# Optimization experiments

Hardware: AMD Instinct MI355X
Metric: run time of the kernel (lower is better)

The kernel has to match this reference:

```python
import jax, jax.numpy as jnp
import numpy as np
import math

IN_DIM = 3
N_LEVELS = 16
F = 2
LOG2_T = 19
T = 2 ** LOG2_T
BASE_RES = 16
FINEST_RES = 512
N_POINTS = 1048576

# Per-level resolutions (static, matches torch buffer construction)
_b = math.exp((math.log(FINEST_RES) - math.log(BASE_RES)) / max(N_LEVELS - 1, 1))
RES = np.array([int(BASE_RES * _b ** i) for i in range(N_LEVELS)], dtype=np.int32)  # [L]
# XOR spatial-hash primes (dim 0 uses prime 1)
PRIMES = np.array([1, 2654435761, 805459861, 3674653429], dtype=np.uint32)


def _hash(coords_u32):
    """coords_u32: (..., IN_DIM) uint32 -> int32 hash in [0, T).
    uint32 wraparound arithmetic gives the same low-19 bits as torch's int64
    math, since T divides 2**32 and XOR/product low bits are self-contained."""
    h = coords_u32[..., 0]
    for d in range(1, IN_DIM):
        h = h ^ (coords_u32[..., d] * PRIMES[d % len(PRIMES)])
    return (h & jnp.uint32(T - 1)).astype(jnp.int32)


def setup_inputs() -> dict:
    key = jax.random.key(0)
    k1, k2 = jax.random.split(key)
    x = jax.random.uniform(k1, (N_POINTS, IN_DIM), dtype=jnp.float32)  # coords in [0,1]
    embeddings = jax.random.uniform(
        k2, (N_LEVELS, T, F), minval=-1e-4, maxval=1e-4, dtype=jnp.float32
    )
    return {"x": x, "embeddings": embeddings}


def reference(x, embeddings):
    N = x.shape[0]
    res_f = jnp.asarray(RES, dtype=x.dtype)            # [L]
    res_i = jnp.asarray(RES, dtype=jnp.int32)          # [L]

    # Scale all levels at once: [L, N, D]
    x_scaled = x[None, :, :] * (res_f[:, None, None] - 1.0)
    x_floor = jnp.clip(x_scaled.astype(jnp.int32), 0, res_i[:, None, None] - 2)
    x_frac = x_scaled - x_floor.astype(x.dtype)        # [L, N, D]

    feat = jnp.zeros((N_LEVELS, N, F), dtype=x.dtype)
    for corner in range(2 ** IN_DIM):                  # fixed 8 corners
        off = np.array([(corner >> d) & 1 for d in range(IN_DIM)], dtype=np.int32)
        corner_coords = jnp.clip(x_floor + off, 0, res_i[:, None, None] - 1)
        h = _hash(corner_coords.astype(jnp.uint32))    # [L, N]
        # gather per-level features: embeddings[l, h[l, n]] -> [L, N, F]
        corner_feat = jnp.take_along_axis(embeddings, h[:, :, None], axis=1)
        # N-linear weight: prod over dims of frac or (1-frac)
        w = jnp.prod(
            jnp.where(off.astype(bool), x_frac, 1.0 - x_frac),
            axis=-1, keepdims=True,
        )                                              # [L, N, 1]
        feat = feat + w * corner_feat

    # concat levels along feature dim: [N, L*F]
    return jnp.moveaxis(feat, 0, 1).reshape(N, N_LEVELS * F)
```

## Files before the change

### kernel.cpp

```cpp
#include <hip/hip_runtime.h>
#include <math.h>
#include <stdint.h>

#define LOG2_T 19
#define T_SIZE (1u << LOG2_T)
#define T_MASK (T_SIZE - 1u)
#define N_LEVELS 16
#define N_DENSE 8
#define PRIME1 2654435761u
#define PRIME2 805459861u

typedef unsigned long long u64;
typedef float f4v __attribute__((ext_vector_type(4)));

struct Params {
    int res[N_LEVELS];
    int brick[N_DENSE];
    int off[N_DENSE];
    int dense_total;
};

__device__ __forceinline__ float bf_lo(uint32_t v) { return __uint_as_float(v << 16); }
__device__ __forceinline__ float bf_hi(uint32_t v) { return __uint_as_float(v & 0xFFFF0000u); }

__device__ __forceinline__ uint32_t f32_to_bf16_rne(float f) {
    uint32_t u = __float_as_uint(f);
    u += 0x7FFFu + ((u >> 16) & 1u);
    return u >> 16;
}
__device__ __forceinline__ uint32_t pack2(float2 e) {
    return f32_to_bf16_rne(e.x) | (f32_to_bf16_rne(e.y) << 16);
}

__device__ __forceinline__ void nt_store_f2(float2 v, float2* p) {
    union { float2 f; u64 u; } cv; cv.f = v;
    __builtin_nontemporal_store(cv.u, (u64*)p);
}
__device__ __forceinline__ float2 nt_load_f2(const float2* p) {
    union { float2 f; u64 u; } cv;
    cv.u = __builtin_nontemporal_load((const u64*)p);
    return cv.f;
}

__device__ __forceinline__ void pair_load(const uint32_t* __restrict__ t,
                                          uint32_t h0, uint32_t& e0, uint32_t& e1) {
    const uint2 q = *(const uint2*)(t + (h0 & ~1u));
    const bool hi = (h0 & 1u);
    e0 = hi ? q.y : q.x;
    e1 = hi ? q.x : q.y;
}

__global__ __launch_bounds__(256) void hg_build_fine(
    const float2* __restrict__ emb, uint32_t* __restrict__ tabF)
{
    const int i = blockIdx.x * 256 + threadIdx.x;
    tabF[i] = pack2(emb[(size_t)N_DENSE * T_SIZE + i]);
}

__global__ __launch_bounds__(256) void hg_build_dense(
    const float2* __restrict__ emb, uint32_t* __restrict__ tabD, Params P)
{
    const int i = blockIdx.x * 256 + threadIdx.x;
    if (i >= P.dense_total) return;
    int l = 0;
    while (l < N_DENSE - 1 && i >= P.off[l + 1]) ++l;
    const int e = i - P.off[l];
    const int B = P.brick[l], R = P.res[l];
    const int sub = e & 7, br = e >> 3;
    int bx = br % B; int t2 = br / B; int by = t2 % B; int bz = t2 / B;
    int x = bx * 2 + (sub & 1);        if (x > R - 1) x = R - 1;
    int y = by * 2 + ((sub >> 1) & 1); if (y > R - 1) y = R - 1;
    int z = bz * 2 + (sub >> 2);       if (z > R - 1) z = R - 1;
    const uint32_t h = ((uint32_t)x ^ ((uint32_t)y * PRIME1) ^ ((uint32_t)z * PRIME2)) & T_MASK;
    tabD[i] = pack2(emb[(size_t)l * T_SIZE + h]);
}

struct Pt { int ix, iy, iz; float fx, fy, fz; };

__device__ __forceinline__ Pt mk_pt(float x0, float x1, float x2,
                                    int rl, float rf) {
    Pt p;
    const float sx = x0 * rf, sy = x1 * rf, sz = x2 * rf;
    int ix = (int)sx; ix = ix < 0 ? 0 : (ix > rl - 2 ? rl - 2 : ix);
    int iy = (int)sy; iy = iy < 0 ? 0 : (iy > rl - 2 ? rl - 2 : iy);
    int iz = (int)sz; iz = iz < 0 ? 0 : (iz > rl - 2 ? rl - 2 : iz);
    p.ix = ix; p.iy = iy; p.iz = iz;
    p.fx = sx - (float)ix; p.fy = sy - (float)iy; p.fz = sz - (float)iz;
    return p;
}

__device__ __forceinline__ void gather_fine(const uint32_t* __restrict__ t,
                                            const Pt& p, uint32_t c[8]) {
    const uint32_t hx0 = (uint32_t)p.ix;
    const uint32_t hy0 = (uint32_t)p.iy * PRIME1, hy1 = hy0 + PRIME1;
    const uint32_t hz0 = (uint32_t)p.iz * PRIME2, hz1 = hz0 + PRIME2;
    const uint32_t n00 = hy0 ^ hz0, n10 = hy1 ^ hz0, n01 = hy0 ^ hz1, n11 = hy1 ^ hz1;
    if ((p.ix & 1) == 0) {
        pair_load(t, (hx0 ^ n00) & T_MASK, c[0], c[1]);
        pair_load(t, (hx0 ^ n10) & T_MASK, c[2], c[3]);
        pair_load(t, (hx0 ^ n01) & T_MASK, c[4], c[5]);
        pair_load(t, (hx0 ^ n11) & T_MASK, c[6], c[7]);
    } else {
        const uint32_t hx1 = hx0 + 1u;
        c[0] = t[(hx0 ^ n00) & T_MASK]; c[1] = t[(hx1 ^ n00) & T_MASK];
        c[2] = t[(hx0 ^ n10) & T_MASK]; c[3] = t[(hx1 ^ n10) & T_MASK];
        c[4] = t[(hx0 ^ n01) & T_MASK]; c[5] = t[(hx1 ^ n01) & T_MASK];
        c[6] = t[(hx0 ^ n11) & T_MASK]; c[7] = t[(hx1 ^ n11) & T_MASK];
    }
}

__device__ __forceinline__ void gather_dense(const uint32_t* __restrict__ t,
                                             int B, const Pt& p, uint32_t c[8]) {
    const int ix = p.ix, iy = p.iy, iz = p.iz;
    const int bx0 = ix >> 1, sx0 = ix & 1;
    const int by0 = iy >> 1, sy0 = iy & 1, by1 = (iy + 1) >> 1, sy1 = (iy + 1) & 1;
    const int bz0 = iz >> 1, sz0 = iz & 1, bz1 = (iz + 1) >> 1, sz1 = (iz + 1) & 1;
    const int zy00 = (((bz0 * B + by0) * B) << 3) | (sy0 << 1) | (sz0 << 2);
    const int zy10 = (((bz0 * B + by1) * B) << 3) | (sy1 << 1) | (sz0 << 2);
    const int zy01 = (((bz1 * B + by0) * B) << 3) | (sy0 << 1) | (sz1 << 2);
    const int zy11 = (((bz1 * B + by1) * B) << 3) | (sy1 << 1) | (sz1 << 2);
    if (sx0 == 0) {
        if (sy0 == 0) {
            const uint4 q0 = *(const uint4*)(t + zy00 + (bx0 << 3));
            const uint4 q1 = *(const uint4*)(t + zy01 + (bx0 << 3));
            c[0] = q0.x; c[1] = q0.y; c[2] = q0.z; c[3] = q0.w;
            c[4] = q1.x; c[5] = q1.y; c[6] = q1.z; c[7] = q1.w;
        } else {
            const uint2 q0 = *(const uint2*)(t + zy00 + (bx0 << 3));
            const uint2 q1 = *(const uint2*)(t + zy10 + (bx0 << 3));
            const uint2 q2 = *(const uint2*)(t + zy01 + (bx0 << 3));
            const uint2 q3 = *(const uint2*)(t + zy11 + (bx0 << 3));
            c[0] = q0.x; c[1] = q0.y; c[2] = q1.x; c[3] = q1.y;
            c[4] = q2.x; c[5] = q2.y; c[6] = q3.x; c[7] = q3.y;
        }
    } else {
        const int bx1 = bx0 + 1;
        c[0] = t[zy00 + (bx0 << 3) + 1]; c[1] = t[zy00 + (bx1 << 3)];
        c[2] = t[zy10 + (bx0 << 3) + 1]; c[3] = t[zy10 + (bx1 << 3)];
        c[4] = t[zy01 + (bx0 << 3) + 1]; c[5] = t[zy01 + (bx1 << 3)];
        c[6] = t[zy11 + (bx0 << 3) + 1]; c[7] = t[zy11 + (bx1 << 3)];
    }
}

__device__ __forceinline__ float2 blend8(const uint32_t c[8], const Pt& p) {
    const float wx0 = 1.0f - p.fx, wx1 = p.fx;
    const float wy0 = 1.0f - p.fy, wy1 = p.fy;
    const float wz0 = 1.0f - p.fz, wz1 = p.fz;
    float w, f0 = 0.0f, f1 = 0.0f;
    w = wx0 * wy0 * wz0; f0 = fmaf(w, bf_lo(c[0]), f0); f1 = fmaf(w, bf_hi(c[0]), f1);
    w = wx1 * wy0 * wz0; f0 = fmaf(w, bf_lo(c[1]), f0); f1 = fmaf(w, bf_hi(c[1]), f1);
    w = wx0 * wy1 * wz0; f0 = fmaf(w, bf_lo(c[2]), f0); f1 = fmaf(w, bf_hi(c[2]), f1);
    w = wx1 * wy1 * wz0; f0 = fmaf(w, bf_lo(c[3]), f0); f1 = fmaf(w, bf_hi(c[3]), f1);
    w = wx0 * wy0 * wz1; f0 = fmaf(w, bf_lo(c[4]), f0); f1 = fmaf(w, bf_hi(c[4]), f1);
    w = wx1 * wy0 * wz1; f0 = fmaf(w, bf_lo(c[5]), f0); f1 = fmaf(w, bf_hi(c[5]), f1);
    w = wx0 * wy1 * wz1; f0 = fmaf(w, bf_lo(c[6]), f0); f1 = fmaf(w, bf_hi(c[6]), f1);
    w = wx1 * wy1 * wz1; f0 = fmaf(w, bf_lo(c[7]), f0); f1 = fmaf(w, bf_hi(c[7]), f1);
    float2 o; o.x = f0; o.y = f1;
    return o;
}

__global__ __launch_bounds__(256, 4) void hg_levels(
    const float* __restrict__ x,
    const uint32_t* __restrict__ tabF,
    const uint32_t* __restrict__ tabD,
    float2* __restrict__ feat,
    int N, Params P)
{
    const int l  = blockIdx.x & 7;
    const int lf = l + 8;
    const int n0 = (blockIdx.x >> 3) * 512 + threadIdx.x;
    if (n0 >= N) return;
    const int n1 = n0 + 256;
    const bool hasB = (n1 < N);
    const int nB = hasB ? n1 : n0;

    const float xa0 = x[n0 * 3 + 0], xa1 = x[n0 * 3 + 1], xa2 = x[n0 * 3 + 2];
    const float xb0 = x[nB * 3 + 0], xb1 = x[nB * 3 + 1], xb2 = x[nB * 3 + 2];

    const int   rd  = P.res[l];  const float rdf = (float)(rd - 1);
    const int   rfi = P.res[lf]; const float rff = (float)(rfi - 1);

    const Pt fA = mk_pt(xa0, xa1, xa2, rfi, rff);
    const Pt fB = mk_pt(xb0, xb1, xb2, rfi, rff);
    const Pt dA = mk_pt(xa0, xa1, xa2, rd, rdf);
    const Pt dB = mk_pt(xb0, xb1, xb2, rd, rdf);

    uint32_t cfA[8], cfB[8], cdA[8], cdB[8];
    const uint32_t* __restrict__ tf = tabF + (size_t)l * T_SIZE;
    gather_fine(tf, fA, cfA);
    gather_fine(tf, fB, cfB);
    const uint32_t* __restrict__ td = tabD + P.off[l];
    const int B = P.brick[l];
    gather_dense(td, B, dA, cdA);
    gather_dense(td, B, dB, cdB);

    __builtin_amdgcn_sched_barrier(0);

    const float2 oFA = blend8(cfA, fA);
    const float2 oFB = blend8(cfB, fB);
    const float2 oDA = blend8(cdA, dA);
    const float2 oDB = blend8(cdB, dB);

    nt_store_f2(oDA, &feat[(size_t)l  * N + n0]);
    nt_store_f2(oFA, &feat[(size_t)lf * N + n0]);
    if (hasB) {
        nt_store_f2(oDB, &feat[(size_t)l  * N + n1]);
        nt_store_f2(oFB, &feat[(size_t)lf * N + n1]);
    }
}

__global__ __launch_bounds__(256) void hg_transpose(
    const float2* __restrict__ feat, f4v* __restrict__ out, int N)
{
    __shared__ float2 st[N_LEVELS][33];
    const int base = blockIdx.x * 32;
    const int t = threadIdx.x;
#pragma unroll
    for (int i = 0; i < 2; ++i) {
        const int idx = i * 256 + t;
        const int l = idx >> 5, p = idx & 31;
        const int n = base + p;
        st[l][p] = (n < N) ? nt_load_f2(&feat[(size_t)l * N + n]) : make_float2(0.f, 0.f);
    }
    __syncthreads();
    const int p = t >> 3, k = t & 7;
    const int n = base + p;
    if (n < N) {
        const float2 a = st[2 * k][p], b = st[2 * k + 1][p];
        f4v o; o.x = a.x; o.y = a.y; o.z = b.x; o.w = b.y;
        __builtin_nontemporal_store(o, &out[(size_t)n * 8 + k]);
    }
}

__global__ __launch_bounds__(256) void hg_fallback(
    const float* __restrict__ x, const float* __restrict__ emb,
    float* __restrict__ out, int N, Params P)
{
    const int gid = blockIdx.x * 256 + threadIdx.x;
    const int n = gid >> 4, l = gid & 15;
    if (n >= N) return;
    const int rl = P.res[l];
    const float rf = (float)(rl - 1);
    float sx = x[n * 3 + 0] * rf, sy = x[n * 3 + 1] * rf, sz = x[n * 3 + 2] * rf;
    int ix = (int)sx; ix = ix < 0 ? 0 : (ix > rl - 2 ? rl - 2 : ix);
    int iy = (int)sy; iy = iy < 0 ? 0 : (iy > rl - 2 ? rl - 2 : iy);
    int iz = (int)sz; iz = iz < 0 ? 0 : (iz > rl - 2 ? rl - 2 : iz);
    const float fx = sx - ix, fy = sy - iy, fz = sz - iz;
    const uint32_t hx0 = (uint32_t)ix, hx1 = hx0 + 1u;
    const uint32_t hy0 = (uint32_t)iy * PRIME1, hy1 = hy0 + PRIME1;
    const uint32_t hz0 = (uint32_t)iz * PRIME2, hz1 = hz0 + PRIME2;
    const float2* tab = (const float2*)emb + (size_t)l * T_SIZE;
    float2 e0 = tab[(hx0 ^ hy0 ^ hz0) & T_MASK], e1 = tab[(hx1 ^ hy0 ^ hz0) & T_MASK];
    float2 e2 = tab[(hx0 ^ hy1 ^ hz0) & T_MASK], e3 = tab[(hx1 ^ hy1 ^ hz0) & T_MASK];
    float2 e4 = tab[(hx0 ^ hy0 ^ hz1) & T_MASK], e5 = tab[(hx1 ^ hy0 ^ hz1) & T_MASK];
    float2 e6 = tab[(hx0 ^ hy1 ^ hz1) & T_MASK], e7 = tab[(hx1 ^ hy1 ^ hz1) & T_MASK];
    const float wx0 = 1.0f - fx, wx1 = fx, wy0 = 1.0f - fy, wy1 = fy, wz0 = 1.0f - fz, wz1 = fz;
    float w, f0 = 0.0f, f1 = 0.0f;
    w = wx0 * wy0 * wz0; f0 = fmaf(w, e0.x, f0); f1 = fmaf(w, e0.y, f1);
    w = wx1 * wy0 * wz0; f0 = fmaf(w, e1.x, f0); f1 = fmaf(w, e1.y, f1);
    w = wx0 * wy1 * wz0; f0 = fmaf(w, e2.x, f0); f1 = fmaf(w, e2.y, f1);
    w = wx1 * wy1 * wz0; f0 = fmaf(w, e3.x, f0); f1 = fmaf(w, e3.y, f1);
    w = wx0 * wy0 * wz1; f0 = fmaf(w, e4.x, f0); f1 = fmaf(w, e4.y, f1);
    w = wx1 * wy0 * wz1; f0 = fmaf(w, e5.x, f0); f1 = fmaf(w, e5.y, f1);
    w = wx0 * wy1 * wz1; f0 = fmaf(w, e6.x, f0); f1 = fmaf(w, e6.y, f1);
    w = wx1 * wy1 * wz1; f0 = fmaf(w, e7.x, f0); f1 = fmaf(w, e7.y, f1);
    float2 o; o.x = f0; o.y = f1;
    ((float2*)out)[(size_t)n * N_LEVELS + l] = o;
}

extern "C" void kernel_launch(void* const* d_in, const int* in_sizes, int n_in,
                              void* d_out, int out_size, void* d_ws, size_t ws_size,
                              hipStream_t stream) {
    const float* x   = (const float*)d_in[0];
    const float* emb = (const float*)d_in[1];
    const int N = in_sizes[0] / 3;

    Params P;
    const double b = exp((log(512.0) - log(16.0)) / 15.0);
    for (int i = 0; i < N_LEVELS; ++i)
        P.res[i] = (int)(16.0 * pow(b, (double)i));
    int acc = 0;
    for (int i = 0; i < N_DENSE; ++i) {
        P.brick[i] = (P.res[i] + 1) >> 1;
        P.off[i] = acc;
        acc += P.brick[i] * P.brick[i] * P.brick[i] * 8;
    }
    P.dense_total = acc;

    const size_t fine_bytes  = (size_t)N_DENSE * T_SIZE * sizeof(uint32_t);
    const size_t dense_bytes = ((size_t)acc * sizeof(uint32_t) + 255) & ~255ull;
    const size_t feat_bytes  = (size_t)N_LEVELS * N * sizeof(float2);

    if (ws_size >= fine_bytes + dense_bytes + feat_bytes) {
        uint32_t* tabF = (uint32_t*)d_ws;
        uint32_t* tabD = (uint32_t*)((char*)d_ws + fine_bytes);
        float2*   feat = (float2*)((char*)d_ws + fine_bytes + dense_bytes);

        hipLaunchKernelGGL(hg_build_fine, dim3(N_DENSE * T_SIZE / 256), dim3(256), 0, stream,
                           (const float2*)emb, tabF);
        hipLaunchKernelGGL(hg_build_dense, dim3((P.dense_total + 255) / 256), dim3(256), 0, stream,
                           (const float2*)emb, tabD, P);

        const int chunks = (N + 511) / 512;
        hipLaunchKernelGGL(hg_levels, dim3(chunks * 8), dim3(256), 0, stream,
                           x, tabF, tabD, feat, N, P);

        hipLaunchKernelGGL(hg_transpose, dim3((N + 31) / 32), dim3(256), 0, stream,
                           feat, (f4v*)d_out, N);
    } else {
        hipLaunchKernelGGL(hg_fallback, dim3((N * 16 + 255) / 256), dim3(256), 0, stream,
                           x, emb, (float*)d_out, N, P);
    }
}
```

Measured before the change: 519.0 us.

## Use per-cell and x-pair dense tables, quad-aligned hashed loads, vectorized I/O

Replaces the 2x2x2 brick dense layout with two schemes. The five coarsest levels store all 8 corners per cell contiguously, so each point needs two 16-byte loads. The next three levels store x-adjacent pairs per row, so each point needs four 8-byte loads. Fine hashed levels now load an aligned uint4 around each hash and pull the x+1 neighbour from it when the XOR delta stays inside the quad, with separate scalar loads otherwise. Each thread now handles two adjacent points, so x loads and feature stores become vectorized. The cost is larger precomputed tables (about 8x duplication for coarse levels) and an extra build kernel.

```diff
diff --git a/kernel.cpp b/kernel.cpp
--- a/kernel.cpp
+++ b/kernel.cpp
@@ -7,6 +7,7 @@
 #define T_MASK (T_SIZE - 1u)
 #define N_LEVELS 16
 #define N_DENSE 8
+#define N_CELL 5
 #define PRIME1 2654435761u
 #define PRIME2 805459861u
 
@@ -15,9 +16,11 @@
 
 struct Params {
     int res[N_LEVELS];
-    int brick[N_DENSE];
-    int off[N_DENSE];
-    int dense_total;
+    int dOff[N_DENSE];
+    int cellOffC[N_CELL + 1];
+    int pairOffE[4];
+    int cellTot;
+    int pairTot;
 };
 
 __device__ __forceinline__ float bf_lo(uint32_t v) { return __uint_as_float(v << 16); }
@@ -42,12 +45,10 @@
     return cv.f;
 }
 
-__device__ __forceinline__ void pair_load(const uint32_t* __restrict__ t,
-                                          uint32_t h0, uint32_t& e0, uint32_t& e1) {
-    const uint2 q = *(const uint2*)(t + (h0 & ~1u));
-    const bool hi = (h0 & 1u);
-    e0 = hi ? q.y : q.x;
-    e1 = hi ? q.x : q.y;
+__device__ __forceinline__ uint32_t sel4(uint4 q, uint32_t s) {
+    const uint32_t a = (s & 1u) ? q.y : q.x;
+    const uint32_t b = (s & 1u) ? q.w : q.z;
+    return (s & 2u) ? b : a;
 }
 
 __global__ __launch_bounds__(256) void hg_build_fine(
@@ -57,22 +58,42 @@
     tabF[i] = pack2(emb[(size_t)N_DENSE * T_SIZE + i]);
 }
 
-__global__ __launch_bounds__(256) void hg_build_dense(
+__global__ __launch_bounds__(256) void hg_build_cell(
     const float2* __restrict__ emb, uint32_t* __restrict__ tabD, Params P)
 {
     const int i = blockIdx.x * 256 + threadIdx.x;
-    if (i >= P.dense_total) return;
+    if (i >= P.cellTot * 8) return;
+    const int cg = i >> 3, k = i & 7;
     int l = 0;
-    while (l < N_DENSE - 1 && i >= P.off[l + 1]) ++l;
-    const int e = i - P.off[l];
-    const int B = P.brick[l], R = P.res[l];
-    const int sub = e & 7, br = e >> 3;
-    int bx = br % B; int t2 = br / B; int by = t2 % B; int bz = t2 / B;
-    int x = bx * 2 + (sub & 1);        if (x > R - 1) x = R - 1;
-    int y = by * 2 + ((sub >> 1) & 1); if (y > R - 1) y = R - 1;
-    int z = bz * 2 + (sub >> 2);       if (z > R - 1) z = R - 1;
-    const uint32_t h = ((uint32_t)x ^ ((uint32_t)y * PRIME1) ^ ((uint32_t)z * PRIME2)) & T_MASK;
-    tabD[i] = pack2(emb[(size_t)l * T_SIZE + h]);
+    while (l < N_CELL - 1 && cg >= P.cellOffC[l + 1]) ++l;
+    const int e = cg - P.cellOffC[l];
+    const int C = P.res[l] - 1;
+    const int ix = e % C; const int r = e / C; const int iy = r % C; const int iz = r / C;
+    const uint32_t xx = (uint32_t)(ix + (k & 1));
+    const uint32_t yy = (uint32_t)(iy + ((k >> 1) & 1));
+    const uint32_t zz = (uint32_t)(iz + (k >> 2));
+    const uint32_t h = (xx ^ (yy * PRIME1) ^ (zz * PRIME2)) & T_MASK;
+    tabD[P.dOff[l] + e * 8 + k] = pack2(emb[(size_t)l * T_SIZE + h]);
+}
+
+__global__ __launch_bounds__(256) void hg_build_pair(
+    const float2* __restrict__ emb, uint32_t* __restrict__ tabD, Params P)
+{
+    const int j = blockIdx.x * 256 + threadIdx.x;
+    if (j >= P.pairTot) return;
+    int lp = 0;
+    while (lp < 2 && j >= P.pairOffE[lp + 1]) ++lp;
+    const int e = j - P.pairOffE[lp];
+    const int l = lp + N_CELL;
+    const int R = P.res[l], C = R - 1;
+    const int ix = e % C; const int r = e / C; const int yc = r % R; const int zc = r / R;
+    const uint32_t m = (((uint32_t)yc) * PRIME1) ^ (((uint32_t)zc) * PRIME2);
+    const uint32_t h0 = (((uint32_t)ix)      ^ m) & T_MASK;
+    const uint32_t h1 = (((uint32_t)ix + 1u) ^ m) & T_MASK;
+    uint2 v;
+    v.x = pack2(emb[(size_t)l * T_SIZE + h0]);
+    v.y = pack2(emb[(size_t)l * T_SIZE + h1]);
+    *(uint2*)(tabD + P.dOff[l] + (size_t)e * 2) = v;
 }
 
 struct Pt { int ix, iy, iz; float fx, fy, fz; };
@@ -89,72 +110,23 @@
     return p;
 }
 
-__device__ __forceinline__ void gather_fine(const uint32_t* __restrict__ t,
-                                            const Pt& p, uint32_t c[8]) {
-    const uint32_t hx0 = (uint32_t)p.ix;
-    const uint32_t hy0 = (uint32_t)p.iy * PRIME1, hy1 = hy0 + PRIME1;
-    const uint32_t hz0 = (uint32_t)p.iz * PRIME2, hz1 = hz0 + PRIME2;
-    const uint32_t n00 = hy0 ^ hz0, n10 = hy1 ^ hz0, n01 = hy0 ^ hz1, n11 = hy1 ^ hz1;
-    if ((p.ix & 1) == 0) {
-        pair_load(t, (hx0 ^ n00) & T_MASK, c[0], c[1]);
-        pair_load(t, (hx0 ^ n10) & T_MASK, c[2], c[3]);
-        pair_load(t, (hx0 ^ n01) & T_MASK, c[4], c[5]);
-        pair_load(t, (hx0 ^ n11) & T_MASK, c[6], c[7]);
-    } else {
-        const uint32_t hx1 = hx0 + 1u;
-        c[0] = t[(hx0 ^ n00) & T_MASK]; c[1] = t[(hx1 ^ n00) & T_MASK];
-        c[2] = t[(hx0 ^ n10) & T_MASK]; c[3] = t[(hx1 ^ n10) & T_MASK];
-        c[4] = t[(hx0 ^ n01) & T_MASK]; c[5] = t[(hx1 ^ n01) & T_MASK];
-        c[6] = t[(hx0 ^ n11) & T_MASK]; c[7] = t[(hx1 ^ n11) & T_MASK];
-    }
-}
-
-__device__ __forceinline__ void gather_dense(const uint32_t* __restrict__ t,
-                                             int B, const Pt& p, uint32_t c[8]) {
-    const int ix = p.ix, iy = p.iy, iz = p.iz;
-    const int bx0 = ix >> 1, sx0 = ix & 1;
-    const int by0 = iy >> 1, sy0 = iy & 1, by1 = (iy + 1) >> 1, sy1 = (iy + 1) & 1;
-    const int bz0 = iz >> 1, sz0 = iz & 1, bz1 = (iz + 1) >> 1, sz1 = (iz + 1) & 1;
-    const int zy00 = (((bz0 * B + by0) * B) << 3) | (sy0 << 1) | (sz0 << 2);
-    const int zy10 = (((bz0 * B + by1) * B) << 3) | (sy1 << 1) | (sz0 << 2);
-    const int zy01 = (((bz1 * B + by0) * B) << 3) | (sy0 << 1) | (sz1 << 2);
-    const int zy11 = (((bz1 * B + by1) * B) << 3) | (sy1 << 1) | (sz1 << 2);
-    if (sx0 == 0) {
-        if (sy0 == 0) {
-            const uint4 q0 = *(const uint4*)(t + zy00 + (bx0 << 3));
-            const uint4 q1 = *(const uint4*)(t + zy01 + (bx0 << 3));
-            c[0] = q0.x; c[1] = q0.y; c[2] = q0.z; c[3] = q0.w;
-            c[4] = q1.x; c[5] = q1.y; c[6] = q1.z; c[7] = q1.w;
-        } else {
-            const uint2 q0 = *(const uint2*)(t + zy00 + (bx0 << 3));
-            const uint2 q1 = *(const uint2*)(t + zy10 + (bx0 << 3));
-            const uint2 q2 = *(const uint2*)(t + zy01 + (bx0 << 3));
-            const uint2 q3 = *(const uint2*)(t + zy11 + (bx0 << 3));
-            c[0] = q0.x; c[1] = q0.y; c[2] = q1.x; c[3] = q1.y;
-            c[4] = q2.x; c[5] = q2.y; c[6] = q3.x; c[7] = q3.y;
-        }
-    } else {
-        const int bx1 = bx0 + 1;
-        c[0] = t[zy00 + (bx0 << 3) + 1]; c[1] = t[zy00 + (bx1 << 3)];
-        c[2] = t[zy10 + (bx0 << 3) + 1]; c[3] = t[zy10 + (bx1 << 3)];
-        c[4] = t[zy01 + (bx0 << 3) + 1]; c[5] = t[zy01 + (bx1 << 3)];
-        c[6] = t[zy11 + (bx0 << 3) + 1]; c[7] = t[zy11 + (bx1 << 3)];
-    }
-}
-
-__device__ __forceinline__ float2 blend8(const uint32_t c[8], const Pt& p) {
-    const float wx0 = 1.0f - p.fx, wx1 = p.fx;
-    const float wy0 = 1.0f - p.fy, wy1 = p.fy;
-    const float wz0 = 1.0f - p.fz, wz1 = p.fz;
+__device__ __forceinline__ float2 blend8s(
+    uint32_t c0, uint32_t c1, uint32_t c2, uint32_t c3,
+    uint32_t c4, uint32_t c5, uint32_t c6, uint32_t c7,
+    float fx, float fy, float fz)
+{
+    const float wx0 = 1.0f - fx, wx1 = fx;
+    const float wy0 = 1.0f - fy, wy1 = fy;
+    const float wz0 = 1.0f - fz, wz1 = fz;
     float w, f0 = 0.0f, f1 = 0.0f;
-    w = wx0 * wy0 * wz0; f0 = fmaf(w, bf_lo(c[0]), f0); f1 = fmaf(w, bf_hi(c[0]), f1);
-    w = wx1 * wy0 * wz0; f0 = fmaf(w, bf_lo(c[1]), f0); f1 = fmaf(w, bf_hi(c[1]), f1);
-    w = wx0 * wy1 * wz0; f0 = fmaf(w, bf_lo(c[2]), f0); f1 = fmaf(w, bf_hi(c[2]), f1);
-    w = wx1 * wy1 * wz0; f0 = fmaf(w, bf_lo(c[3]), f0); f1 = fmaf(w, bf_hi(c[3]), f1);
-    w = wx0 * wy0 * wz1; f0 = fmaf(w, bf_lo(c[4]), f0); f1 = fmaf(w, bf_hi(c[4]), f1);
-    w = wx1 * wy0 * wz1; f0 = fmaf(w, bf_lo(c[5]), f0); f1 = fmaf(w, bf_hi(c[5]), f1);
-    w = wx0 * wy1 * wz1; f0 = fmaf(w, bf_lo(c[6]), f0); f1 = fmaf(w, bf_hi(c[6]), f1);
-    w = wx1 * wy1 * wz1; f0 = fmaf(w, bf_lo(c[7]), f0); f1 = fmaf(w, bf_hi(c[7]), f1);
+    w = wx0 * wy0 * wz0; f0 = fmaf(w, bf_lo(c0), f0); f1 = fmaf(w, bf_hi(c0), f1);
+    w = wx1 * wy0 * wz0; f0 = fmaf(w, bf_lo(c1), f0); f1 = fmaf(w, bf_hi(c1), f1);
+    w = wx0 * wy1 * wz0; f0 = fmaf(w, bf_lo(c2), f0); f1 = fmaf(w, bf_hi(c2), f1);
+    w = wx1 * wy1 * wz0; f0 = fmaf(w, bf_lo(c3), f0); f1 = fmaf(w, bf_hi(c3), f1);
+    w = wx0 * wy0 * wz1; f0 = fmaf(w, bf_lo(c4), f0); f1 = fmaf(w, bf_hi(c4), f1);
+    w = wx1 * wy0 * wz1; f0 = fmaf(w, bf_lo(c5), f0); f1 = fmaf(w, bf_hi(c5), f1);
+    w = wx0 * wy1 * wz1; f0 = fmaf(w, bf_lo(c6), f0); f1 = fmaf(w, bf_hi(c6), f1);
+    w = wx1 * wy1 * wz1; f0 = fmaf(w, bf_lo(c7), f0); f1 = fmaf(w, bf_hi(c7), f1);
     float2 o; o.x = f0; o.y = f1;
     return o;
 }
@@ -168,44 +140,148 @@
 {
     const int l  = blockIdx.x & 7;
     const int lf = l + 8;
-    const int n0 = (blockIdx.x >> 3) * 512 + threadIdx.x;
+    const int tt = (blockIdx.x >> 3) * 256 + threadIdx.x;
+    const int n0 = tt * 2;
     if (n0 >= N) return;
-    const int n1 = n0 + 256;
+    const int n1 = n0 + 1;
     const bool hasB = (n1 < N);
-    const int nB = hasB ? n1 : n0;
-
-    const float xa0 = x[n0 * 3 + 0], xa1 = x[n0 * 3 + 1], xa2 = x[n0 * 3 + 2];
-    const float xb0 = x[nB * 3 + 0], xb1 = x[nB * 3 + 1], xb2 = x[nB * 3 + 2];
-
-    const int   rd  = P.res[l];  const float rdf = (float)(rd - 1);
-    const int   rfi = P.res[lf]; const float rff = (float)(rfi - 1);
-
-    const Pt fA = mk_pt(xa0, xa1, xa2, rfi, rff);
-    const Pt fB = mk_pt(xb0, xb1, xb2, rfi, rff);
-    const Pt dA = mk_pt(xa0, xa1, xa2, rd, rdf);
-    const Pt dB = mk_pt(xb0, xb1, xb2, rd, rdf);
-
-    uint32_t cfA[8], cfB[8], cdA[8], cdB[8];
+
+    float ax, ay, az, bx, by, bz;
+    const float* xb = x + (size_t)n0 * 3;
+    if (hasB) {
+        const float2 u0 = *(const float2*)(xb);
+        const float2 u1 = *(const float2*)(xb + 2);
+        const float2 u2 = *(const float2*)(xb + 4);
+        ax = u0.x; ay = u0.y; az = u1.x; bx = u1.y; by = u2.x; bz = u2.y;
+    } else {
+        ax = xb[0]; ay = xb[1]; az = xb[2]; bx = ax; by = ay; bz = az;
+    }
+
+    const int rd = P.res[l];  const float rdf = (float)(rd - 1);
+    const int rf = P.res[lf]; const float rff = (float)(rf - 1);
+
+    const Pt fA = mk_pt(ax, ay, az, rf, rff);
+    const Pt fB = mk_pt(bx, by, bz, rf, rff);
+    const Pt dA = mk_pt(ax, ay, az, rd, rdf);
+    const Pt dB = mk_pt(bx, by, bz, rd, rdf);
+
     const uint32_t* __restrict__ tf = tabF + (size_t)l * T_SIZE;
-    gather_fine(tf, fA, cfA);
-    gather_fine(tf, fB, cfB);
-    const uint32_t* __restrict__ td = tabD + P.off[l];
-    const int B = P.brick[l];
-    gather_dense(td, B, dA, cdA);
-    gather_dense(td, B, dB, cdB);
+
+    const uint32_t hxA = (uint32_t)fA.ix;
+    const uint32_t dxA = hxA ^ (hxA + 1u);
+    const uint32_t yA0 = (uint32_t)fA.iy * PRIME1, yA1 = yA0 + PRIME1;
+    const uint32_t zA0 = (uint32_t)fA.iz * PRIME2, zA1 = zA0 + PRIME2;
+    const uint32_t iA00 = (hxA ^ yA0 ^ zA0) & T_MASK;
+    const uint32_t iA10 = (hxA ^ yA1 ^ zA0) & T_MASK;
+    const uint32_t iA01 = (hxA ^ yA0 ^ zA1) & T_MASK;
+    const uint32_t iA11 = (hxA ^ yA1 ^ zA1) & T_MASK;
+    const uint4 qA00 = *(const uint4*)(tf + (iA00 & ~3u));
+    const uint4 qA10 = *(const uint4*)(tf + (iA10 & ~3u));
+    const uint4 qA01 = *(const uint4*)(tf + (iA01 & ~3u));
+    const uint4 qA11 = *(const uint4*)(tf + (iA11 & ~3u));
+
+    const uint32_t hxB = (uint32_t)fB.ix;
+    const uint32_t dxB = hxB ^ (hxB + 1u);
+    const uint32_t yB0 = (uint32_t)fB.iy * PRIME1, yB1 = yB0 + PRIME1;
+    const uint32_t zB0 = (uint32_t)fB.iz * PRIME2, zB1 = zB0 + PRIME2;
+    const uint32_t iB00 = (hxB ^ yB0 ^ zB0) & T_MASK;
+    const uint32_t iB10 = (hxB ^ yB1 ^ zB0) & T_MASK;
+    const uint32_t iB01 = (hxB ^ yB0 ^ zB1) & T_MASK;
+    const uint32_t iB11 = (hxB ^ yB1 ^ zB1) & T_MASK;
+    const uint4 qB00 = *(const uint4*)(tf + (iB00 & ~3u));
+    const uint4 qB10 = *(const uint4*)(tf + (iB10 & ~3u));
+    const uint4 qB01 = *(const uint4*)(tf + (iB01 & ~3u));
+    const uint4 qB11 = *(const uint4*)(tf + (iB11 & ~3u));
+
+    uint32_t eA1 = 0, eA3 = 0, eA5 = 0, eA7 = 0;
+    const bool exA = dxA >= 4u;
+    if (exA) {
+        eA1 = tf[(iA00 ^ dxA) & T_MASK];
+        eA3 = tf[(iA10 ^ dxA) & T_MASK];
+        eA5 = tf[(iA01 ^ dxA) & T_MASK];
+        eA7 = tf[(iA11 ^ dxA) & T_MASK];
+    }
+    uint32_t eB1 = 0, eB3 = 0, eB5 = 0, eB7 = 0;
+    const bool exB = dxB >= 4u;
+    if (exB) {
+        eB1 = tf[(iB00 ^ dxB) & T_MASK];
+        eB3 = tf[(iB10 ^ dxB) & T_MASK];
+        eB5 = tf[(iB01 ^ dxB) & T_MASK];
+        eB7 = tf[(iB11 ^ dxB) & T_MASK];
+    }
+
+    uint32_t a0, a1, a2, a3, a4, a5, a6, a7;
+    uint32_t b0, b1, b2, b3, b4, b5, b6, b7;
+    if (l < N_CELL) {
+        const int C = rd - 1;
+        const uint32_t* cbA = tabD + P.dOff[l] + (size_t)((dA.iz * C + dA.iy) * C + dA.ix) * 8;
+        const uint4 qa0 = *(const uint4*)cbA;
+        const uint4 qa1 = *(const uint4*)(cbA + 4);
+        const uint32_t* cbB = tabD + P.dOff[l] + (size_t)((dB.iz * C + dB.iy) * C + dB.ix) * 8;
+        const uint4 qb0 = *(const uint4*)cbB;
+        const uint4 qb1 = *(const uint4*)(cbB + 4);
+        a0 = qa0.x; a1 = qa0.y; a2 = qa0.z; a3 = qa0.w;
+        a4 = qa1.x; a5 = qa1.y; a6 = qa1.z; a7 = qa1.w;
+        b0 = qb0.x; b1 = qb0.y; b2 = qb0.z; b3 = qb0.w;
+        b4 = qb1.x; b5 = qb1.y; b6 = qb1.z; b7 = qb1.w;
+    } else {
+        const int R = rd, C = rd - 1;
+        const uint32_t* pb = tabD + P.dOff[l];
+        const int rA0 = (dA.iz * R + dA.iy) * C + dA.ix;
+        const int rA1 = rA0 + C;
+        const int rA2 = rA0 + R * C;
+        const int rA3 = rA2 + C;
+        const uint2 pA0 = *(const uint2*)(pb + (size_t)rA0 * 2);
+        const uint2 pA1 = *(const uint2*)(pb + (size_t)rA1 * 2);
+        const uint2 pA2 = *(const uint2*)(pb + (size_t)rA2 * 2);
+        const uint2 pA3 = *(const uint2*)(pb + (size_t)rA3 * 2);
+        const int rB0 = (dB.iz * R + dB.iy) * C + dB.ix;
+        const int rB1 = rB0 + C;
+        const int rB2 = rB0 + R * C;
+        const int rB3 = rB2 + C;
+        const uint2 pB0 = *(const uint2*)(pb + (size_t)rB0 * 2);
+        const uint2 pB1 = *(const uint2*)(pb + (size_t)rB1 * 2);
+        const uint2 pB2 = *(const uint2*)(pb + (size_t)rB2 * 2);
+        const uint2 pB3 = *(const uint2*)(pb + (size_t)rB3 * 2);
+        a0 = pA0.x; a1 = pA0.y; a2 = pA1.x; a3 = pA1.y;
+        a4 = pA2.x; a5 = pA2.y; a6 = pA3.x; a7 = pA3.y;
+        b0 = pB0.x; b1 = pB0.y; b2 = pB1.x; b3 = pB1.y;
+        b4 = pB2.x; b5 = pB2.y; b6 = pB3.x; b7 = pB3.y;
+    }
 
     __builtin_amdgcn_sched_barrier(0);
 
-    const float2 oFA = blend8(cfA, fA);
-    const float2 oFB = blend8(cfB, fB);
-    const float2 oDA = blend8(cdA, dA);
-    const float2 oDB = blend8(cdB, dB);
-
-    nt_store_f2(oDA, &feat[(size_t)l  * N + n0]);
-    nt_store_f2(oFA, &feat[(size_t)lf * N + n0]);
+    const uint32_t fA0 = sel4(qA00, iA00 & 3u);
+    const uint32_t fA1 = exA ? eA1 : sel4(qA00, (iA00 ^ dxA) & 3u);
+    const uint32_t fA2 = sel4(qA10, iA10 & 3u);
+    const uint32_t fA3 = exA ? eA3 : sel4(qA10, (iA10 ^ dxA) & 3u);
+    const uint32_t fA4 = sel4(qA01, iA01 & 3u);
+    const uint32_t fA5 = exA ? eA5 : sel4(qA01, (iA01 ^ dxA) & 3u);
+    const uint32_t fA6 = sel4(qA11, iA11 & 3u);
+    const uint32_t fA7 = exA ? eA7 : sel4(qA11, (iA11 ^ dxA) & 3u);
+
+    const uint32_t fB0 = sel4(qB00, iB00 & 3u);
+    const uint32_t fB1 = exB ? eB1 : sel4(qB00, (iB00 ^ dxB) & 3u);
+    const uint32_t fB2 = sel4(qB10, iB10 & 3u);
+    const uint32_t fB3 = exB ? eB3 : sel4(qB10, (iB10 ^ dxB) & 3u);
+    const uint32_t fB4 = sel4(qB01, iB01 & 3u);
+    const uint32_t fB5 = exB ? eB5 : sel4(qB01, (iB01 ^ dxB) & 3u);
+    const uint32_t fB6 = sel4(qB11, iB11 & 3u);
+    const uint32_t fB7 = exB ? eB7 : sel4(qB11, (iB11 ^ dxB) & 3u);
+
+    const float2 oFA = blend8s(fA0, fA1, fA2, fA3, fA4, fA5, fA6, fA7, fA.fx, fA.fy, fA.fz);
+    const float2 oFB = blend8s(fB0, fB1, fB2, fB3, fB4, fB5, fB6, fB7, fB.fx, fB.fy, fB.fz);
+    const float2 oDA = blend8s(a0, a1, a2, a3, a4, a5, a6, a7, dA.fx, dA.fy, dA.fz);
+    const float2 oDB = blend8s(b0, b1, b2, b3, b4, b5, b6, b7, dB.fx, dB.fy, dB.fz);
+
     if (hasB) {
-        nt_store_f2(oDB, &feat[(size_t)l  * N + n1]);
-        nt_store_f2(oFB, &feat[(size_t)lf * N + n1]);
+        f4v oD; oD.x = oDA.x; oD.y = oDA.y; oD.z = oDB.x; oD.w = oDB.y;
+        __builtin_nontemporal_store(oD, (f4v*)&feat[(size_t)l * N + n0]);
+        f4v oF; oF.x = oFA.x; oF.y = oFA.y; oF.z = oFB.x; oF.w = oFB.y;
+        __builtin_nontemporal_store(oF, (f4v*)&feat[(size_t)lf * N + n0]);
+    } else {
+        nt_store_f2(oDA, &feat[(size_t)l  * N + n0]);
+        nt_store_f2(oFA, &feat[(size_t)lf * N + n0]);
     }
 }
 
@@ -279,16 +355,25 @@
     const double b = exp((log(512.0) - log(16.0)) / 15.0);
     for (int i = 0; i < N_LEVELS; ++i)
         P.res[i] = (int)(16.0 * pow(b, (double)i));
-    int acc = 0;
-    for (int i = 0; i < N_DENSE; ++i) {
-        P.brick[i] = (P.res[i] + 1) >> 1;
-        P.off[i] = acc;
-        acc += P.brick[i] * P.brick[i] * P.brick[i] * 8;
-    }
-    P.dense_total = acc;
+
+    P.cellOffC[0] = 0;
+    for (int l = 0; l < N_CELL; ++l) {
+        const int C = P.res[l] - 1;
+        P.cellOffC[l + 1] = P.cellOffC[l] + C * C * C;
+    }
+    P.cellTot = P.cellOffC[N_CELL];
+    P.pairOffE[0] = 0;
+    for (int lp = 0; lp < 3; ++lp) {
+        const int R = P.res[N_CELL + lp], C = R - 1;
+        P.pairOffE[lp + 1] = P.pairOffE[lp] + C * R * R;
+    }
+    P.pairTot = P.pairOffE[3];
+    for (int l = 0; l < N_CELL; ++l) P.dOff[l] = P.cellOffC[l] * 8;
+    for (int lp = 0; lp < 3; ++lp)  P.dOff[N_CELL + lp] = P.cellTot * 8 + P.pairOffE[lp] * 2;
+    const size_t dense_dwords = (size_t)P.cellTot * 8 + (size_t)P.pairTot * 2;
 
     const size_t fine_bytes  = (size_t)N_DENSE * T_SIZE * sizeof(uint32_t);
-    const size_t dense_bytes = ((size_t)acc * sizeof(uint32_t) + 255) & ~255ull;
+    const size_t dense_bytes = (dense_dwords * sizeof(uint32_t) + 255) & ~255ull;
     const size_t feat_bytes  = (size_t)N_LEVELS * N * sizeof(float2);
 
     if (ws_size >= fine_bytes + dense_bytes + feat_bytes) {
@@ -298,7 +383,9 @@
 
         hipLaunchKernelGGL(hg_build_fine, dim3(N_DENSE * T_SIZE / 256), dim3(256), 0, stream,
                            (const float2*)emb, tabF);
-        hipLaunchKernelGGL(hg_build_dense, dim3((P.dense_total + 255) / 256), dim3(256), 0, stream,
+        hipLaunchKernelGGL(hg_build_cell, dim3((P.cellTot * 8 + 255) / 256), dim3(256), 0, stream,
+                           (const float2*)emb, tabD, P);
+        hipLaunchKernelGGL(hg_build_pair, dim3((P.pairTot + 255) / 256), dim3(256), 0, stream,
                            (const float2*)emb, tabD, P);
 
         const int chunks = (N + 511) / 512;
```

After: 614.3 us. +18.4%, slower.

## Replace brick dense tables with per-cell corner tables and quad-aligned hash gathers

Applied to the files above, without the earlier changes.

Only the coarsest 5 levels now get a dense table, and it stores all 8 corners of each cell contiguously, so a cell lookup is two 16-byte loads. The remaining 11 levels use a bf16 hash table read with 16-byte aligned quad loads that often cover both x-neighbours. Each thread now handles two adjacent points, which allows vectorised loads of x and 16-byte stores of features. The transpose tile grows to 128 points per block. The per-cell table duplicates corners about 8x and makes the build kernel larger, while the hash levels trade more bytes per load for fewer loads.

```diff
diff --git a/kernel.cpp b/kernel.cpp
--- a/kernel.cpp
+++ b/kernel.cpp
@@ -6,7 +6,8 @@
 #define T_SIZE (1u << LOG2_T)
 #define T_MASK (T_SIZE - 1u)
 #define N_LEVELS 16
-#define N_DENSE 8
+#define N_CELL 5
+#define N_HASH 11
 #define PRIME1 2654435761u
 #define PRIME2 805459861u
 
@@ -15,9 +16,9 @@
 
 struct Params {
     int res[N_LEVELS];
-    int brick[N_DENSE];
-    int off[N_DENSE];
-    int dense_total;
+    int dOff[N_CELL];
+    int cellOffC[N_CELL + 1];
+    int cellTot;
 };
 
 __device__ __forceinline__ float bf_lo(uint32_t v) { return __uint_as_float(v << 16); }
@@ -32,47 +33,45 @@
     return f32_to_bf16_rne(e.x) | (f32_to_bf16_rne(e.y) << 16);
 }
 
-__device__ __forceinline__ void nt_store_f2(float2 v, float2* p) {
-    union { float2 f; u64 u; } cv; cv.f = v;
-    __builtin_nontemporal_store(cv.u, (u64*)p);
-}
 __device__ __forceinline__ float2 nt_load_f2(const float2* p) {
     union { float2 f; u64 u; } cv;
     cv.u = __builtin_nontemporal_load((const u64*)p);
     return cv.f;
 }
-
-__device__ __forceinline__ void pair_load(const uint32_t* __restrict__ t,
-                                          uint32_t h0, uint32_t& e0, uint32_t& e1) {
-    const uint2 q = *(const uint2*)(t + (h0 & ~1u));
-    const bool hi = (h0 & 1u);
-    e0 = hi ? q.y : q.x;
-    e1 = hi ? q.x : q.y;
+__device__ __forceinline__ void nt_store_f2(float2 v, float2* p) {
+    union { float2 f; u64 u; } cv; cv.f = v;
+    __builtin_nontemporal_store(cv.u, (u64*)p);
+}
+
+__device__ __forceinline__ uint32_t sel4(uint4 q, uint32_t s) {
+    const uint32_t a = (s & 1u) ? q.y : q.x;
+    const uint32_t b = (s & 1u) ? q.w : q.z;
+    return (s & 2u) ? b : a;
 }
 
 __global__ __launch_bounds__(256) void hg_build_fine(
     const float2* __restrict__ emb, uint32_t* __restrict__ tabF)
 {
     const int i = blockIdx.x * 256 + threadIdx.x;
-    tabF[i] = pack2(emb[(size_t)N_DENSE * T_SIZE + i]);
-}
-
-__global__ __launch_bounds__(256) void hg_build_dense(
+    tabF[i] = pack2(emb[(size_t)N_CELL * T_SIZE + i]);
+}
+
+__global__ __launch_bounds__(256) void hg_build_cell(
     const float2* __restrict__ emb, uint32_t* __restrict__ tabD, Params P)
 {
     const int i = blockIdx.x * 256 + threadIdx.x;
-    if (i >= P.dense_total) return;
+    if (i >= P.cellTot * 8) return;
+    const int cg = i >> 3, k = i & 7;
     int l = 0;
-    while (l < N_DENSE - 1 && i >= P.off[l + 1]) ++l;
-    const int e = i - P.off[l];
-    const int B = P.brick[l], R = P.res[l];
-    const int sub = e & 7, br = e >> 3;
-    int bx = br % B; int t2 = br / B; int by = t2 % B; int bz = t2 / B;
-    int x = bx * 2 + (sub & 1);        if (x > R - 1) x = R - 1;
-    int y = by * 2 + ((sub >> 1) & 1); if (y > R - 1) y = R - 1;
-    int z = bz * 2 + (sub >> 2);       if (z > R - 1) z = R - 1;
-    const uint32_t h = ((uint32_t)x ^ ((uint32_t)y * PRIME1) ^ ((uint32_t)z * PRIME2)) & T_MASK;
-    tabD[i] = pack2(emb[(size_t)l * T_SIZE + h]);
+    while (l < N_CELL - 1 && cg >= P.cellOffC[l + 1]) ++l;
+    const int e = cg - P.cellOffC[l];
+    const int C = P.res[l] - 1;
+    const int ix = e % C; const int r = e / C; const int iy = r % C; const int iz = r / C;
+    const uint32_t xx = (uint32_t)(ix + (k & 1));
+    const uint32_t yy = (uint32_t)(iy + ((k >> 1) & 1));
+    const uint32_t zz = (uint32_t)(iz + (k >> 2));
+    const uint32_t h = (xx ^ (yy * PRIME1) ^ (zz * PRIME2)) & T_MASK;
+    tabD[P.dOff[l] + e * 8 + k] = pack2(emb[(size_t)l * T_SIZE + h]);
 }
 
 struct Pt { int ix, iy, iz; float fx, fy, fz; };
@@ -89,72 +88,65 @@
     return p;
 }
 
-__device__ __forceinline__ void gather_fine(const uint32_t* __restrict__ t,
-                                            const Pt& p, uint32_t c[8]) {
-    const uint32_t hx0 = (uint32_t)p.ix;
-    const uint32_t hy0 = (uint32_t)p.iy * PRIME1, hy1 = hy0 + PRIME1;
-    const uint32_t hz0 = (uint32_t)p.iz * PRIME2, hz1 = hz0 + PRIME2;
-    const uint32_t n00 = hy0 ^ hz0, n10 = hy1 ^ hz0, n01 = hy0 ^ hz1, n11 = hy1 ^ hz1;
-    if ((p.ix & 1) == 0) {
-        pair_load(t, (hx0 ^ n00) & T_MASK, c[0], c[1]);
-        pair_load(t, (hx0 ^ n10) & T_MASK, c[2], c[3]);
-        pair_load(t, (hx0 ^ n01) & T_MASK, c[4], c[5]);
-        pair_load(t, (hx0 ^ n11) & T_MASK, c[6], c[7]);
-    } else {
-        const uint32_t hx1 = hx0 + 1u;
-        c[0] = t[(hx0 ^ n00) & T_MASK]; c[1] = t[(hx1 ^ n00) & T_MASK];
-        c[2] = t[(hx0 ^ n10) & T_MASK]; c[3] = t[(hx1 ^ n10) & T_MASK];
-        c[4] = t[(hx0 ^ n01) & T_MASK]; c[5] = t[(hx1 ^ n01) & T_MASK];
-        c[6] = t[(hx0 ^ n11) & T_MASK]; c[7] = t[(hx1 ^ n11) & T_MASK];
-    }
-}
-
-__device__ __forceinline__ void gather_dense(const uint32_t* __restrict__ t,
-                                             int B, const Pt& p, uint32_t c[8]) {
-    const int ix = p.ix, iy = p.iy, iz = p.iz;
-    const int bx0 = ix >> 1, sx0 = ix & 1;
-    const int by0 = iy >> 1, sy0 = iy & 1, by1 = (iy + 1) >> 1, sy1 = (iy + 1) & 1;
-    const int bz0 = iz >> 1, sz0 = iz & 1, bz1 = (iz + 1) >> 1, sz1 = (iz + 1) & 1;
-    const int zy00 = (((bz0 * B + by0) * B) << 3) | (sy0 << 1) | (sz0 << 2);
-    const int zy10 = (((bz0 * B + by1) * B) << 3) | (sy1 << 1) | (sz0 << 2);
-    const int zy01 = (((bz1 * B + by0) * B) << 3) | (sy0 << 1) | (sz1 << 2);
-    const int zy11 = (((bz1 * B + by1) * B) << 3) | (sy1 << 1) | (sz1 << 2);
-    if (sx0 == 0) {
-        if (sy0 == 0) {
-            const uint4 q0 = *(const uint4*)(t + zy00 + (bx0 << 3));
-            const uint4 q1 = *(const uint4*)(t + zy01 + (bx0 << 3));
-            c[0] = q0.x; c[1] = q0.y; c[2] = q0.z; c[3] = q0.w;
-            c[4] = q1.x; c[5] = q1.y; c[6] = q1.z; c[7] = q1.w;
-        } else {
-            const uint2 q0 = *(const uint2*)(t + zy00 + (bx0 << 3));
-            const uint2 q1 = *(const uint2*)(t + zy10 + (bx0 << 3));
-            const uint2 q2 = *(const uint2*)(t + zy01 + (bx0 << 3));
-            const uint2 q3 = *(const uint2*)(t + zy11 + (bx0 << 3));
-            c[0] = q0.x; c[1] = q0.y; c[2] = q1.x; c[3] = q1.y;
-            c[4] = q2.x; c[5] = q2.y; c[6] = q3.x; c[7] = q3.y;
-        }
-    } else {
-        const int bx1 = bx0 + 1;
-        c[0] = t[zy00 + (bx0 << 3) + 1]; c[1] = t[zy00 + (bx1 << 3)];
-        c[2] = t[zy10 + (bx0 << 3) + 1]; c[3] = t[zy10 + (bx1 << 3)];
-        c[4] = t[zy01 + (bx0 << 3) + 1]; c[5] = t[zy01 + (bx1 << 3)];
-        c[6] = t[zy11 + (bx0 << 3) + 1]; c[7] = t[zy11 + (bx1 << 3)];
-    }
-}
-
-__device__ __forceinline__ float2 blend8(const uint32_t c[8], const Pt& p) {
+struct C8 { uint32_t c0, c1, c2, c3, c4, c5, c6, c7; };
+
+__device__ __forceinline__ C8 gather_hash(const uint32_t* __restrict__ t,
+                                          const Pt& p) {
+    const uint32_t hx = (uint32_t)p.ix;
+    const uint32_t dx = hx ^ (hx + 1u);
+    const uint32_t y0 = (uint32_t)p.iy * PRIME1, y1 = y0 + PRIME1;
+    const uint32_t z0 = (uint32_t)p.iz * PRIME2, z1 = z0 + PRIME2;
+    const uint32_t i00 = (hx ^ y0 ^ z0) & T_MASK;
+    const uint32_t i10 = (hx ^ y1 ^ z0) & T_MASK;
+    const uint32_t i01 = (hx ^ y0 ^ z1) & T_MASK;
+    const uint32_t i11 = (hx ^ y1 ^ z1) & T_MASK;
+    const uint4 q00 = *(const uint4*)(t + (i00 & ~3u));
+    const uint4 q10 = *(const uint4*)(t + (i10 & ~3u));
+    const uint4 q01 = *(const uint4*)(t + (i01 & ~3u));
+    const uint4 q11 = *(const uint4*)(t + (i11 & ~3u));
+    C8 r;
+    if (dx < 4u) {
+        r.c1 = sel4(q00, (i00 ^ dx) & 3u);
+        r.c3 = sel4(q10, (i10 ^ dx) & 3u);
+        r.c5 = sel4(q01, (i01 ^ dx) & 3u);
+        r.c7 = sel4(q11, (i11 ^ dx) & 3u);
+    } else {
+        r.c1 = t[(i00 ^ dx) & T_MASK];
+        r.c3 = t[(i10 ^ dx) & T_MASK];
+        r.c5 = t[(i01 ^ dx) & T_MASK];
+        r.c7 = t[(i11 ^ dx) & T_MASK];
+    }
+    r.c0 = sel4(q00, i00 & 3u);
+    r.c2 = sel4(q10, i10 & 3u);
+    r.c4 = sel4(q01, i01 & 3u);
+    r.c6 = sel4(q11, i11 & 3u);
+    return r;
+}
+
+__device__ __forceinline__ C8 gather_cell(const uint32_t* __restrict__ t,
+                                          int C, const Pt& p) {
+    const uint32_t* cb = t + (size_t)((p.iz * C + p.iy) * C + p.ix) * 8;
+    const uint4 q0 = *(const uint4*)cb;
+    const uint4 q1 = *(const uint4*)(cb + 4);
+    C8 r;
+    r.c0 = q0.x; r.c1 = q0.y; r.c2 = q0.z; r.c3 = q0.w;
+    r.c4 = q1.x; r.c5 = q1.y; r.c6 = q1.z; r.c7 = q1.w;
+    return r;
+}
+
+__device__ __forceinline__ float2 blend8(const C8& c, const Pt& p) {
     const float wx0 = 1.0f - p.fx, wx1 = p.fx;
     const float wy0 = 1.0f - p.fy, wy1 = p.fy;
     const float wz0 = 1.0f - p.fz, wz1 = p.fz;
     float w, f0 = 0.0f, f1 = 0.0f;
-    w = wx0 * wy0 * wz0; f0 = fmaf(w, bf_lo(c[0]), f0); f1 = fmaf(w, bf_hi(c[0]), f1);
-    w = wx1 * wy0 * wz0; f0 = fmaf(w, bf_lo(c[1]), f0); f1 = fmaf(w, bf_hi(c[1]), f1);
-    w = wx0 * wy1 * wz0; f0 = fmaf(w, bf_lo(c[2]), f0); f1 = fmaf(w, bf_hi(c[2]), f1);
-    w = wx1 * wy1 * wz0; f0 = fmaf(w, bf_lo(c[3]), f0); f1 = fmaf(w, bf_hi(c[3]), f1);
-    w = wx0 * wy0 * wz1; f0 = fmaf(w, bf_lo(c[4]), f0); f1 = fmaf(w, bf_hi(c[4]), f1);
-    w = wx1 * wy0 * wz1; f0 = fmaf(w, bf_lo(c[5]), f0); f1 = fmaf(w, bf_hi(c[5]), f1);
-    w = wx0 * wy1 * wz1; f0 = fmaf(w, bf_lo(c[6]), f0); f1 = fmaf(w, bf_hi(c[6]), f1);
-    w = wx1 * wy1 * wz1; f0 = fmaf(w, bf_lo(c[7]), f0); f1 = fmaf(w, bf_hi(c[7]), f1);
+    w = wx0 * wy0 * wz0; f0 = fmaf(w, bf_lo(c.c0), f0); f1 = fmaf(w, bf_hi(c.c0), f1);
+    w = wx1 * wy0 * wz0; f0 = fmaf(w, bf_lo(c.c1), f0); f1 = fmaf(w, bf_hi(c.c1), f1);
+    w = wx0 * wy1 * wz0; f0 = fmaf(w, bf_lo(c.c2), f0); f1 = fmaf(w, bf_hi(c.c2), f1);
+    w = wx1 * wy1 * wz0; f0 = fmaf(w, bf_lo(c.c3), f0); f1 = fmaf(w, bf_hi(c.c3), f1);
+    w = wx0 * wy0 * wz1; f0 = fmaf(w, bf_lo(c.c4), f0); f1 = fmaf(w, bf_hi(c.c4), f1);
+    w = wx1 * wy0 * wz1; f0 = fmaf(w, bf_lo(c.c5), f0); f1 = fmaf(w, bf_hi(c.c5), f1);
+    w = wx0 * wy1 * wz1; f0 = fmaf(w, bf_lo(c.c6), f0); f1 = fmaf(w, bf_hi(c.c6), f1);
+    w = wx1 * wy1 * wz1; f0 = fmaf(w, bf_lo(c.c7), f0); f1 = fmaf(w, bf_hi(c.c7), f1);
     float2 o; o.x = f0; o.y = f1;
     return o;
 }
@@ -168,67 +160,94 @@
 {
     const int l  = blockIdx.x & 7;
     const int lf = l + 8;
-    const int n0 = (blockIdx.x >> 3) * 512 + threadIdx.x;
+    const int tt = (blockIdx.x >> 3) * 256 + threadIdx.x;
+    const int n0 = tt * 2;
     if (n0 >= N) return;
-    const int n1 = n0 + 256;
+    const int n1 = n0 + 1;
     const bool hasB = (n1 < N);
-    const int nB = hasB ? n1 : n0;
-
-    const float xa0 = x[n0 * 3 + 0], xa1 = x[n0 * 3 + 1], xa2 = x[n0 * 3 + 2];
-    const float xb0 = x[nB * 3 + 0], xb1 = x[nB * 3 + 1], xb2 = x[nB * 3 + 2];
-
-    const int   rd  = P.res[l];  const float rdf = (float)(rd - 1);
-    const int   rfi = P.res[lf]; const float rff = (float)(rfi - 1);
-
-    const Pt fA = mk_pt(xa0, xa1, xa2, rfi, rff);
-    const Pt fB = mk_pt(xb0, xb1, xb2, rfi, rff);
-    const Pt dA = mk_pt(xa0, xa1, xa2, rd, rdf);
-    const Pt dB = mk_pt(xb0, xb1, xb2, rd, rdf);
-
-    uint32_t cfA[8], cfB[8], cdA[8], cdB[8];
-    const uint32_t* __restrict__ tf = tabF + (size_t)l * T_SIZE;
-    gather_fine(tf, fA, cfA);
-    gather_fine(tf, fB, cfB);
-    const uint32_t* __restrict__ td = tabD + P.off[l];
-    const int B = P.brick[l];
-    gather_dense(td, B, dA, cdA);
-    gather_dense(td, B, dB, cdB);
-
-    __builtin_amdgcn_sched_barrier(0);
+
+    float ax, ay, az, bx, by, bz;
+    const float* xb = x + (size_t)n0 * 3;
+    if (hasB) {
+        const float2 u0 = *(const float2*)(xb);
+        const float2 u1 = *(const float2*)(xb + 2);
+        const float2 u2 = *(const float2*)(xb + 4);
+        ax = u0.x; ay = u0.y; az = u1.x; bx = u1.y; by = u2.x; bz = u2.y;
+    } else {
+        ax = xb[0]; ay = xb[1]; az = xb[2]; bx = ax; by = ay; bz = az;
+    }
+
+    const int rd = P.res[l];  const float rdf = (float)(rd - 1);
+    const int rh = P.res[lf]; const float rhf = (float)(rh - 1);
+
+    const Pt fA = mk_pt(ax, ay, az, rh, rhf);
+    const Pt fB = mk_pt(bx, by, bz, rh, rhf);
+    const Pt dA = mk_pt(ax, ay, az, rd, rdf);
+    const Pt dB = mk_pt(bx, by, bz, rd, rdf);
+
+    const uint32_t* __restrict__ tfF = tabF + (size_t)(lf - N_CELL) * T_SIZE;
+    const C8 cfA = gather_hash(tfF, fA);
+    const C8 cfB = gather_hash(tfF, fB);
+
+    C8 cdA, cdB;
+    if (l < N_CELL) {
+        const uint32_t* __restrict__ td = tabD + P.dOff[l];
+        const int C = rd - 1;
+        cdA = gather_cell(td, C, dA);
+        cdB = gather_cell(td, C, dB);
+    } else {
+        const uint32_t* __restrict__ tfD = tabF + (size_t)(l - N_CELL) * T_SIZE;
+        cdA = gather_hash(tfD, dA);
+        cdB = gather_hash(tfD, dB);
+    }
 
     const float2 oFA = blend8(cfA, fA);
     const float2 oFB = blend8(cfB, fB);
     const float2 oDA = blend8(cdA, dA);
     const float2 oDB = blend8(cdB, dB);
 
-    nt_store_f2(oDA, &feat[(size_t)l  * N + n0]);
-    nt_store_f2(oFA, &feat[(size_t)lf * N + n0]);
     if (hasB) {
-        nt_store_f2(oDB, &feat[(size_t)l  * N + n1]);
-        nt_store_f2(oFB, &feat[(size_t)lf * N + n1]);
+        f4v oD; oD.x = oDA.x; oD.y = oDA.y; oD.z = oDB.x; oD.w = oDB.y;
+        __builtin_nontemporal_store(oD, (f4v*)&feat[(size_t)l * N + n0]);
+        f4v oF; oF.x = oFA.x; oF.y = oFA.y; oF.z = oFB.x; oF.w = oFB.y;
+        __builtin_nontemporal_store(oF, (f4v*)&feat[(size_t)lf * N + n0]);
+    } else {
+        nt_store_f2(oDA, &feat[(size_t)l  * N + n0]);
+        nt_store_f2(oFA, &feat[(size_t)lf * N + n0]);
     }
 }
 
 __global__ __launch_bounds__(256) void hg_transpose(
     const float2* __restrict__ feat, f4v* __restrict__ out, int N)
 {
-    __shared__ float2 st[N_LEVELS][33];
-    const int base = blockIdx.x * 32;
+    __shared__ float2 st[N_LEVELS][131];
+    const int base = blockIdx.x * 128;
     const int t = threadIdx.x;
 #pragma unroll
-    for (int i = 0; i < 2; ++i) {
+    for (int i = 0; i < 4; ++i) {
         const int idx = i * 256 + t;
-        const int l = idx >> 5, p = idx & 31;
+        const int l = idx >> 6, pp = (idx & 63) * 2;
+        const int n = base + pp;
+        float2 v0 = make_float2(0.f, 0.f), v1 = v0;
+        if (n + 1 < N) {
+            const f4v q = __builtin_nontemporal_load((const f4v*)&feat[(size_t)l * N + n]);
+            v0.x = q.x; v0.y = q.y; v1.x = q.z; v1.y = q.w;
+        } else if (n < N) {
+            v0 = nt_load_f2(&feat[(size_t)l * N + n]);
+        }
+        st[l][pp] = v0; st[l][pp + 1] = v1;
+    }
+    __syncthreads();
+#pragma unroll
+    for (int i = 0; i < 4; ++i) {
+        const int idx = i * 256 + t;
+        const int p = idx >> 3, k = idx & 7;
         const int n = base + p;
-        st[l][p] = (n < N) ? nt_load_f2(&feat[(size_t)l * N + n]) : make_float2(0.f, 0.f);
-    }
-    __syncthreads();
-    const int p = t >> 3, k = t & 7;
-    const int n = base + p;
-    if (n < N) {
-        const float2 a = st[2 * k][p], b = st[2 * k + 1][p];
-        f4v o; o.x = a.x; o.y = a.y; o.z = b.x; o.w = b.y;
-        __builtin_nontemporal_store(o, &out[(size_t)n * 8 + k]);
+        if (n < N) {
+            const float2 a = st[2 * k][p], b = st[2 * k + 1][p];
+            f4v o; o.x = a.x; o.y = a.y; o.z = b.x; o.w = b.y;
+            __builtin_nontemporal_store(o, &out[(size_t)n * 8 + k]);
+        }
     }
 }
 
@@ -279,16 +298,17 @@
     const double b = exp((log(512.0) - log(16.0)) / 15.0);
     for (int i = 0; i < N_LEVELS; ++i)
         P.res[i] = (int)(16.0 * pow(b, (double)i));
-    int acc = 0;
-    for (int i = 0; i < N_DENSE; ++i) {
-        P.brick[i] = (P.res[i] + 1) >> 1;
-        P.off[i] = acc;
-        acc += P.brick[i] * P.brick[i] * P.brick[i] * 8;
-    }
-    P.dense_total = acc;
-
-    const size_t fine_bytes  = (size_t)N_DENSE * T_SIZE * sizeof(uint32_t);
-    const size_t dense_bytes = ((size_t)acc * sizeof(uint32_t) + 255) & ~255ull;
+
+    P.cellOffC[0] = 0;
+    for (int l = 0; l < N_CELL; ++l) {
+        const int C = P.res[l] - 1;
+        P.cellOffC[l + 1] = P.cellOffC[l] + C * C * C;
+    }
+    P.cellTot = P.cellOffC[N_CELL];
+    for (int l = 0; l < N_CELL; ++l) P.dOff[l] = P.cellOffC[l] * 8;
+
+    const size_t fine_bytes  = (size_t)N_HASH * T_SIZE * sizeof(uint32_t);
+    const size_t dense_bytes = ((size_t)P.cellTot * 8 * sizeof(uint32_t) + 255) & ~255ull;
     const size_t feat_bytes  = (size_t)N_LEVELS * N * sizeof(float2);
 
     if (ws_size >= fine_bytes + dense_bytes + feat_bytes) {
@@ -296,16 +316,16 @@
         uint32_t* tabD = (uint32_t*)((char*)d_ws + fine_bytes);
         float2*   feat = (float2*)((char*)d_ws + fine_bytes + dense_bytes);
 
-        hipLaunchKernelGGL(hg_build_fine, dim3(N_DENSE * T_SIZE / 256), dim3(256), 0, stream,
+        hipLaunchKernelGGL(hg_build_fine, dim3(N_HASH * T_SIZE / 256), dim3(256), 0, stream,
                            (const float2*)emb, tabF);
-        hipLaunchKernelGGL(hg_build_dense, dim3((P.dense_total + 255) / 256), dim3(256), 0, stream,
+        hipLaunchKernelGGL(hg_build_cell, dim3((P.cellTot * 8 + 255) / 256), dim3(256), 0, stream,
                            (const float2*)emb, tabD, P);
 
         const int chunks = (N + 511) / 512;
         hipLaunchKernelGGL(hg_levels, dim3(chunks * 8), dim3(256), 0, stream,
                            x, tabF, tabD, feat, N, P);
 
-        hipLaunchKernelGGL(hg_transpose, dim3((N + 31) / 32), dim3(256), 0, stream,
+        hipLaunchKernelGGL(hg_transpose, dim3((N + 127) / 128), dim3(256), 0, stream,
                            feat, (f4v*)d_out, N);
     } else {
         hipLaunchKernelGGL(hg_fallback, dim3((N * 16 + 255) / 256), dim3(256), 0, stream,
```

New measurement: 548.3 us. 5.7% more time.
